# Kernel tuning notes

Measured on AMD Instinct MI355X. Metric: run time of the kernel, lower is better.

Reference implementation:

```python
import jax, jax.numpy as jnp
import numpy as np

HID = 128
SCALE = np.sqrt(HID)


def _ln(x, g, b, eps=1e-5):
    m = jnp.mean(x, axis=-1, keepdims=True)
    v = jnp.mean((x - m) ** 2, axis=-1, keepdims=True)
    return (x - m) * jax.lax.rsqrt(v + eps) * g + b


def _attention(img, txt, Wi, bi, Wt, bt, g1, b1, Wq, bq, Wk, bk, Wv, bv, g2, b2, Wo, bo):
    # img: [..., S, image_dim], txt: [..., S, text_dim] -> [..., S, HID]
    c = img @ Wi.T + bi + txt @ Wt.T + bt
    c = _ln(c, g1, b1)
    q = c @ Wq.T + bq
    k = c @ Wk.T + bk
    v = c @ Wv.T + bv
    s = jnp.einsum('...qd,...kd->...qk', q, k) / (SCALE + 1e-8)
    a = jax.nn.softmax(s, axis=-1)
    a = a + 1e-10
    a = a / jnp.sum(a, axis=-1, keepdims=True)
    a = jnp.clip(a, 1e-7, 1.0)
    ctx = jnp.einsum('...qk,...kd->...qd', a, v)
    ctx = _ln(ctx, g2, b2)
    return ctx @ Wo.T + bo


def setup_inputs() -> dict:
    key = jax.random.key(0)
    ks = jax.random.split(key, 24)
    T, Q, DI, DT = 256, 64, 2048, 768

    def xavier(k, shape):
        fan_in, fan_out = shape[1], shape[0]
        lim = np.sqrt(6.0 / (fan_in + fan_out))
        return jax.random.uniform(k, shape, jnp.float32, -lim, lim)

    return {
        'support_images': jax.random.normal(ks[0], (T, 4, DI), jnp.float32),
        'support_texts': jax.random.normal(ks[1], (T, 4, DT), jnp.float32),
        'support_labels': jax.random.randint(ks[2], (T, 4), 0, 4, jnp.int64),
        'query_images': jax.random.normal(ks[3], (T, Q, DI), jnp.float32),
        'query_texts': jax.random.normal(ks[4], (T, Q, DT), jnp.float32),
        'Wi': xavier(ks[5], (HID, DI)), 'bi': jnp.zeros((HID,)),
        'Wt': xavier(ks[6], (HID, DT)), 'bt': jnp.zeros((HID,)),
        'g1': jnp.ones((HID,)), 'b1': jnp.zeros((HID,)),
        'Wq': xavier(ks[7], (HID, HID)), 'bq': jnp.zeros((HID,)),
        'Wk': xavier(ks[8], (HID, HID)), 'bk': jnp.zeros((HID,)),
        'Wv': xavier(ks[9], (HID, HID)), 'bv': jnp.zeros((HID,)),
        'g2': jnp.ones((HID,)), 'b2': jnp.zeros((HID,)),
        'Wo': xavier(ks[10], (HID, HID)), 'bo': jnp.zeros((HID,)),
    }


def reference(support_images, support_texts, support_labels, query_images, query_texts,
              Wi, bi, Wt, bt, g1, b1, Wq, bq, Wk, bk, Wv, bv, g2, b2, Wo, bo):
    p = (Wi, bi, Wt, bt, g1, b1, Wq, bq, Wk, bk, Wv, bv, g2, b2, Wo, bo)
    # Support: attention across the 4 support items of each task -> [T, 4, HID]
    support_feats = _attention(support_images, support_texts, *p)
    # Queries: source processes each query alone (seq len 1) -> add singleton seq axis
    qf = _attention(query_images[:, :, None, :], query_texts[:, :, None, :], *p)
    qf = qf[:, :, 0, :]  # [T, Q, HID]
    # Cosine-similarity prototype scoring (eps=1e-8 as in F.cosine_similarity)
    qn = qf / jnp.clip(jnp.linalg.norm(qf, axis=-1, keepdims=True), 1e-8, None)
    pn = support_feats / jnp.clip(jnp.linalg.norm(support_feats, axis=-1, keepdims=True), 1e-8, None)
    logits = jnp.einsum('tqd,tcd->tqc', qn, pn) * 10.0  # [T, Q, 4]
    return logits
```

## Files before the change

### kernel.cpp

```cpp
#include <hip/hip_runtime.h>

typedef __bf16 bf16_t;
typedef __attribute__((ext_vector_type(4))) __bf16 bf16x4;
typedef __attribute__((ext_vector_type(8))) __bf16 bf16x8;
typedef __attribute__((ext_vector_type(4))) float floatx4;

#define LN_EPS 1e-5f

__device__ __forceinline__ void dma16(const void* g, void* l) {
    __builtin_amdgcn_global_load_lds(
        (const __attribute__((address_space(1))) void*)g,
        (__attribute__((address_space(3))) void*)l, 16, 0, 0);
}

#define WBF_WI 65536
#define WBF_WT (65536 + 262144)

__global__ __launch_bounds__(256) void k0_prep(
    const float* __restrict__ bi, const float* __restrict__ bt,
    const float* __restrict__ Wq, const float* __restrict__ Wk,
    const float* __restrict__ Wv, const float* __restrict__ Wo,
    const float* __restrict__ Wi, const float* __restrict__ Wt,
    float* __restrict__ c_all, bf16_t* __restrict__ wbf)
{
    const int b = blockIdx.x;
    if (b < 2176) {
        int i = b * 256 + threadIdx.x;
        int c4 = i & 31;
        float4 a = ((const float4*)bi)[c4];
        float4 bb = ((const float4*)bt)[c4];
        float4 v; v.x = a.x + bb.x; v.y = a.y + bb.y; v.z = a.z + bb.z; v.w = a.w + bb.w;
        ((float4*)c_all)[i] = v;
    } else {
        int i4 = (b - 2176) * 256 + threadIdx.x;
        const float* src; int dst;
        if (i4 < 16384) {
            int which = i4 >> 12, off4 = i4 & 4095;
            src = ((which == 0) ? Wq : (which == 1) ? Wk : (which == 2) ? Wv : Wo) + off4 * 4;
            dst = which * 16384 + off4 * 4;
        } else if (i4 < 16384 + 65536) {
            int off4 = i4 - 16384;
            src = Wi + off4 * 4; dst = WBF_WI + off4 * 4;
        } else {
            int off4 = i4 - (16384 + 65536);
            src = Wt + off4 * 4; dst = WBF_WT + off4 * 4;
        }
        float4 v = *(const float4*)src;
        bf16x4 pk; pk.x = (bf16_t)v.x; pk.y = (bf16_t)v.y;
                   pk.z = (bf16_t)v.z; pk.w = (bf16_t)v.w;
        *(bf16x4*)&wbf[dst] = pk;
    }
}

#define K1_MFMA8(FA0, FA1)                                                     \
    acc[0][0] = __builtin_amdgcn_mfma_f32_16x16x32_bf16(FA0, fb0, acc[0][0], 0, 0, 0); \
    acc[0][1] = __builtin_amdgcn_mfma_f32_16x16x32_bf16(FA0, fb1, acc[0][1], 0, 0, 0); \
    acc[0][2] = __builtin_amdgcn_mfma_f32_16x16x32_bf16(FA0, fb2, acc[0][2], 0, 0, 0); \
    acc[0][3] = __builtin_amdgcn_mfma_f32_16x16x32_bf16(FA0, fb3, acc[0][3], 0, 0, 0); \
    acc[1][0] = __builtin_amdgcn_mfma_f32_16x16x32_bf16(FA1, fb0, acc[1][0], 0, 0, 0); \
    acc[1][1] = __builtin_amdgcn_mfma_f32_16x16x32_bf16(FA1, fb1, acc[1][1], 0, 0, 0); \
    acc[1][2] = __builtin_amdgcn_mfma_f32_16x16x32_bf16(FA1, fb2, acc[1][2], 0, 0, 0); \
    acc[1][3] = __builtin_amdgcn_mfma_f32_16x16x32_bf16(FA1, fb3, acc[1][3], 0, 0, 0);

#define K1_BODY(A0, A1, B0, B1, B2, B3, K)                                     \
    {                                                                          \
        float4 p00 = *(const float4*)((A0) + (K));                             \
        float4 p01 = *(const float4*)((A0) + (K) + 4);                         \
        float4 p10 = *(const float4*)((A1) + (K));                             \
        float4 p11 = *(const float4*)((A1) + (K) + 4);                         \
        bf16x8 fb0 = *(const bf16x8*)((B0) + (K));                             \
        bf16x8 fb1 = *(const bf16x8*)((B1) + (K));                             \
        bf16x8 fb2 = *(const bf16x8*)((B2) + (K));                             \
        bf16x8 fb3 = *(const bf16x8*)((B3) + (K));                             \
        bf16x8 fa0, fa1;                                                       \
        fa0[0] = (bf16_t)p00.x; fa0[1] = (bf16_t)p00.y;                        \
        fa0[2] = (bf16_t)p00.z; fa0[3] = (bf16_t)p00.w;                        \
        fa0[4] = (bf16_t)p01.x; fa0[5] = (bf16_t)p01.y;                        \
        fa0[6] = (bf16_t)p01.z; fa0[7] = (bf16_t)p01.w;                        \
        fa1[0] = (bf16_t)p10.x; fa1[1] = (bf16_t)p10.y;                        \
        fa1[2] = (bf16_t)p10.z; fa1[3] = (bf16_t)p10.w;                        \
        fa1[4] = (bf16_t)p11.x; fa1[5] = (bf16_t)p11.y;                        \
        fa1[6] = (bf16_t)p11.z; fa1[7] = (bf16_t)p11.w;                        \
        K1_MFMA8(fa0, fa1)                                                     \
    }

__global__ __launch_bounds__(256, 4) void k1_gemm(
    const float* __restrict__ qimg, const float* __restrict__ qtxt,
    const float* __restrict__ simg, const float* __restrict__ stxt,
    const bf16_t* __restrict__ wbf, float* __restrict__ c_all)
{
    const bf16_t* Wib = wbf + WBF_WI;
    const bf16_t* Wtb = wbf + WBF_WT;

    const int tid  = threadIdx.x;
    const int m0   = blockIdx.x * 64;
    const int chnk = blockIdx.y;
    const bool isq = (m0 < 16384);
    const int rb   = isq ? m0 : (m0 - 16384);
    const float* Aimg = isq ? qimg : simg;
    const float* Atxt = isq ? qtxt : stxt;

    const int wid  = tid >> 6;
    const int lane = tid & 63;
    const int quad = lane >> 4;
    const int l16  = lane & 15;
    const int wr   = wid >> 1;
    const int wc   = wid & 1;

    const int ar0 = rb + wr * 32 + l16;
    const int bc0 = wc * 64 + l16;

    floatx4 acc[2][4];
#pragma unroll
    for (int i = 0; i < 2; ++i)
#pragma unroll
        for (int j = 0; j < 4; ++j) acc[i][j] = (floatx4)0.f;

    const int kb = chnk * 704;
    const int ke = kb + 704;

    const int ie = (ke < 2048) ? ke : 2048;
    if (kb < ie) {
        const float*  a0 = Aimg + (size_t)ar0 * 2048 + quad * 8 + kb;
        const float*  a1 = a0 + (size_t)16 * 2048;
        const bf16_t* b0 = Wib + (size_t)bc0 * 2048 + quad * 8 + kb;
        const bf16_t* b1 = b0 + (size_t)16 * 2048;
        const bf16_t* b2 = b0 + (size_t)32 * 2048;
        const bf16_t* b3 = b0 + (size_t)48 * 2048;
        const int n = ie - kb;
#pragma unroll 2
        for (int k = 0; k < n; k += 32) K1_BODY(a0, a1, b0, b1, b2, b3, k)
    }
    const int ts = (kb > 2048) ? kb : 2048;
    if (ts < ke) {
        const int off = ts - 2048;
        const float*  a0 = Atxt + (size_t)ar0 * 768 + quad * 8 + off;
        const float*  a1 = a0 + (size_t)16 * 768;
        const bf16_t* b0 = Wtb + (size_t)bc0 * 768 + quad * 8 + off;
        const bf16_t* b1 = b0 + (size_t)16 * 768;
        const bf16_t* b2 = b0 + (size_t)32 * 768;
        const bf16_t* b3 = b0 + (size_t)48 * 768;
        const int n = ke - ts;
#pragma unroll 2
        for (int k = 0; k < n; k += 32) K1_BODY(a0, a1, b0, b1, b2, b3, k)
    }

#pragma unroll
    for (int nt = 0; nt < 4; ++nt) {
        int col = wc * 64 + nt * 16 + l16;
#pragma unroll
        for (int mt = 0; mt < 2; ++mt)
#pragma unroll
            for (int r = 0; r < 4; ++r) {
                int row = wr * 32 + mt * 16 + quad * 4 + r;
                unsafeAtomicAdd(&c_all[(size_t)(m0 + row) * 128 + col], acc[mt][nt][r]);
            }
    }
}

#define K2_ST 136

__global__ __launch_bounds__(256) void k2_fused(
    const float* __restrict__ c_all, const bf16_t* __restrict__ wbf,
    const float* __restrict__ bq, const float* __restrict__ bk,
    const float* __restrict__ bv, const float* __restrict__ bo,
    const float* __restrict__ g1, const float* __restrict__ b1,
    const float* __restrict__ g2, const float* __restrict__ b2,
    float* __restrict__ out)
{
    __shared__ bf16_t tT[64 * K2_ST];
    __shared__ bf16_t tW[128 * 128];
    __shared__ float  cs[4][128];
    __shared__ float  qkv[3][4][128];
    __shared__ float  att[4][4];
    __shared__ float  pl[4][132];

    const int tid  = threadIdx.x;
    const int wid  = tid >> 6;
    const int lane = tid & 63;
    const int quad = lane >> 4;
    const int l16  = lane & 15;
    const int task = blockIdx.x;
    const int t0   = task * 64;
    const int r0   = wid * 16;
    const int jr4  = lane >> 4;
    const int jp   = lane & 15;

#pragma unroll
    for (int ii = 0; ii < 8; ++ii) {
        int i = 8 * wid + ii;
        int row = 4 * i + jr4;
        int c = jp ^ (row & 15);
        dma16(wbf + 0 * 16384 + row * 128 + c * 8, (char*)tW + i * 1024);
    }

    float bvr[8], g2r[8], b2r[8], bor[8];
#pragma unroll
    for (int nt = 0; nt < 8; ++nt) {
        int col = nt * 16 + l16;
        bvr[nt] = bv[col]; g2r[nt] = g2[col]; b2r[nt] = b2[col]; bor[nt] = bo[col];
    }

    {
        const int g8 = lane >> 3, s8 = lane & 7;
        float g1a[16], b1a[16];
#pragma unroll
        for (int mm = 0; mm < 4; ++mm) {
            *(float4*)&g1a[mm * 4] = ((const float4*)(g1 + s8 * 16))[mm];
            *(float4*)&b1a[mm * 4] = ((const float4*)(b1 + s8 * 16))[mm];
        }
#pragma unroll
        for (int p = 0; p < 2; ++p) {
            int rloc = r0 + p * 8 + g8;
            const float* src = c_all + (size_t)(t0 + rloc) * 128 + s8 * 16;
            float v[16];
#pragma unroll
            for (int mm = 0; mm < 4; ++mm) *(float4*)&v[mm * 4] = ((const float4*)src)[mm];
            float s = 0.f, q = 0.f;
#pragma unroll
            for (int m = 0; m < 16; ++m) { s += v[m]; q += v[m] * v[m]; }
#pragma unroll
            for (int m = 1; m < 8; m <<= 1) { s += __shfl_xor(s, m); q += __shfl_xor(q, m); }
            float mean = s * (1.f / 128.f);
            float var  = q * (1.f / 128.f) - mean * mean;
            float rs   = rsqrtf(var + LN_EPS);
            bf16x8 o0, o1;
#pragma unroll
            for (int m = 0; m < 8; ++m) o0[m] = (bf16_t)((v[m] - mean) * rs * g1a[m] + b1a[m]);
#pragma unroll
            for (int m = 0; m < 8; ++m) o1[m] = (bf16_t)((v[8 + m] - mean) * rs * g1a[8 + m] + b1a[8 + m]);
            *(bf16x8*)&tT[rloc * K2_ST + s8 * 16]     = o0;
            *(bf16x8*)&tT[rloc * K2_ST + s8 * 16 + 8] = o1;
        }
    }
    {
        const float* src = c_all + (size_t)(16384 + task * 4 + wid) * 128;
        float x0 = src[lane], x1 = src[64 + lane];
        float s = x0 + x1, q = x0 * x0 + x1 * x1;
#pragma unroll
        for (int m = 1; m < 64; m <<= 1) { s += __shfl_xor(s, m); q += __shfl_xor(q, m); }
        float mean = s * (1.f / 128.f);
        float var  = q * (1.f / 128.f) - mean * mean;
        float rs   = rsqrtf(var + LN_EPS);
        cs[wid][lane]      = (x0 - mean) * rs * g1[lane] + b1[lane];
        cs[wid][64 + lane] = (x1 - mean) * rs * g1[64 + lane] + b1[64 + lane];
    }
    __syncthreads();

#pragma unroll
    for (int j = 0; j < 2; ++j) {
        int o = tid + j * 256, s = o >> 7, n = o & 127;
        const float4* c4 = (const float4*)cs[s];
        float acc = 0.f;
#pragma unroll
        for (int c = 0; c < 16; ++c) {
            bf16x8 wv = *(const bf16x8*)&tW[n * 128 + ((c ^ (n & 15)) << 3)];
            float4 a0 = c4[c * 2], a1 = c4[c * 2 + 1];
            acc += a0.x * (float)wv[0] + a0.y * (float)wv[1]
                 + a0.z * (float)wv[2] + a0.w * (float)wv[3]
                 + a1.x * (float)wv[4] + a1.y * (float)wv[5]
                 + a1.z * (float)wv[6] + a1.w * (float)wv[7];
        }
        qkv[0][s][n] = acc + bq[n];
    }
    __syncthreads();
#pragma unroll
    for (int ii = 0; ii < 8; ++ii) {
        int i = 8 * wid + ii;
        int row = 4 * i + jr4;
        int c = jp ^ (row & 15);
        dma16(wbf + 1 * 16384 + row * 128 + c * 8, (char*)tW + i * 1024);
    }
    __syncthreads();
#pragma unroll
    for (int j = 0; j < 2; ++j) {
        int o = tid + j * 256, s = o >> 7, n = o & 127;
        const float4* c4 = (const float4*)cs[s];
        float acc = 0.f;
#pragma unroll
        for (int c = 0; c < 16; ++c) {
            bf16x8 wv = *(const bf16x8*)&tW[n * 128 + ((c ^ (n & 15)) << 3)];
            float4 a0 = c4[c * 2], a1 = c4[c * 2 + 1];
            acc += a0.x * (float)wv[0] + a0.y * (float)wv[1]
                 + a0.z * (float)wv[2] + a0.w * (float)wv[3]
                 + a1.x * (float)wv[4] + a1.y * (float)wv[5]
                 + a1.z * (float)wv[6] + a1.w * (float)wv[7];
        }
        qkv[1][s][n] = acc + bk[n];
    }
    __syncthreads();
#pragma unroll
    for (int ii = 0; ii < 8; ++ii) {
        int i = 8 * wid + ii;
        int row = 4 * i + jr4;
        int c = jp ^ (row & 15);
        dma16(wbf + 2 * 16384 + row * 128 + c * 8, (char*)tW + i * 1024);
    }
    __syncthreads();

    floatx4 acc[8];
#pragma unroll
    for (int nt = 0; nt < 8; ++nt) acc[nt] = (floatx4)0.f;
#pragma unroll
    for (int ks = 0; ks < 4; ++ks) {
        bf16x8 a = *(const bf16x8*)&tT[(r0 + l16) * K2_ST + ks * 32 + quad * 8];
#pragma unroll
        for (int nt = 0; nt < 8; ++nt) {
            bf16x8 b = *(const bf16x8*)&tW[(nt * 16 + l16) * 128 + (((ks * 4 + quad) ^ l16) << 3)];
            acc[nt] = __builtin_amdgcn_mfma_f32_16x16x32_bf16(a, b, acc[nt], 0, 0, 0);
        }
    }
#pragma unroll
    for (int nt = 0; nt < 8; ++nt)
#pragma unroll
        for (int r = 0; r < 4; ++r) acc[nt][r] += bvr[nt];

#pragma unroll
    for (int j = 0; j < 2; ++j) {
        int o = tid + j * 256, s = o >> 7, n = o & 127;
        const float4* c4 = (const float4*)cs[s];
        float a = 0.f;
#pragma unroll
        for (int c = 0; c < 16; ++c) {
            bf16x8 wv = *(const bf16x8*)&tW[n * 128 + ((c ^ (n & 15)) << 3)];
            float4 a0 = c4[c * 2], a1 = c4[c * 2 + 1];
            a += a0.x * (float)wv[0] + a0.y * (float)wv[1]
               + a0.z * (float)wv[2] + a0.w * (float)wv[3]
               + a1.x * (float)wv[4] + a1.y * (float)wv[5]
               + a1.z * (float)wv[6] + a1.w * (float)wv[7];
        }
        qkv[2][s][n] = a + bv[n];
    }
    if (tid < 16) {
        int i = tid >> 2, j = tid & 3;
        const float4* qv = (const float4*)qkv[0][i];
        const float4* kv = (const float4*)qkv[1][j];
        float a = 0.f;
#pragma unroll
        for (int k = 0; k < 32; ++k) {
            float4 x = qv[k], y = kv[k];
            a += x.x * y.x + x.y * y.y + x.z * y.z + x.w * y.w;
        }
        att[i][j] = a * (float)(1.0 / (11.313708498984761 + 1e-8));
    }
#pragma unroll
    for (int r = 0; r < 4; ++r) {
        float s = 0.f, q = 0.f;
#pragma unroll
        for (int nt = 0; nt < 8; ++nt) { float x = acc[nt][r]; s += x; q += x * x; }
#pragma unroll
        for (int m = 1; m < 16; m <<= 1) { s += __shfl_xor(s, m); q += __shfl_xor(q, m); }
        float mean = s * (1.f / 128.f);
        float var  = q * (1.f / 128.f) - mean * mean;
        float rs   = rsqrtf(var + LN_EPS);
        int row = r0 + quad * 4 + r;
#pragma unroll
        for (int nt = 0; nt < 8; ++nt)
            tT[row * K2_ST + nt * 16 + l16] = (bf16_t)((acc[nt][r] - mean) * rs * g2r[nt] + b2r[nt]);
    }
    __syncthreads();
#pragma unroll
    for (int ii = 0; ii < 8; ++ii) {
        int i = 8 * wid + ii;
        int row = 4 * i + jr4;
        int c = jp ^ (row & 15);
        dma16(wbf + 3 * 16384 + row * 128 + c * 8, (char*)tW + i * 1024);
    }
    if (tid < 4) {
        float s0 = att[tid][0], s1 = att[tid][1], s2 = att[tid][2], s3 = att[tid][3];
        float m = fmaxf(fmaxf(s0, s1), fmaxf(s2, s3));
        float e0 = expf(s0 - m), e1 = expf(s1 - m), e2 = expf(s2 - m), e3 = expf(s3 - m);
        float se = e0 + e1 + e2 + e3;
        float a0 = e0 / se + 1e-10f, a1 = e1 / se + 1e-10f;
        float a2 = e2 / se + 1e-10f, a3 = e3 / se + 1e-10f;
        float t = a0 + a1 + a2 + a3;
        att[tid][0] = fminf(fmaxf(a0 / t, 1e-7f), 1.f);
        att[tid][1] = fminf(fmaxf(a1 / t, 1e-7f), 1.f);
        att[tid][2] = fminf(fmaxf(a2 / t, 1e-7f), 1.f);
        att[tid][3] = fminf(fmaxf(a3 / t, 1e-7f), 1.f);
    }
    __syncthreads();

#pragma unroll
    for (int j = 0; j < 2; ++j) {
        int o = tid + j * 256, s = o >> 7, n = o & 127;
        qkv[0][s][n] = att[s][0] * qkv[2][0][n] + att[s][1] * qkv[2][1][n]
                     + att[s][2] * qkv[2][2][n] + att[s][3] * qkv[2][3][n];
    }
    __syncthreads();
    {
        float x0 = qkv[0][wid][lane], x1 = qkv[0][wid][64 + lane];
        float s = x0 + x1, q = x0 * x0 + x1 * x1;
#pragma unroll
        for (int m = 1; m < 64; m <<= 1) { s += __shfl_xor(s, m); q += __shfl_xor(q, m); }
        float mean = s * (1.f / 128.f);
        float var  = q * (1.f / 128.f) - mean * mean;
        float rs   = rsqrtf(var + LN_EPS);
        cs[wid][lane]      = (x0 - mean) * rs * g2[lane] + b2[lane];
        cs[wid][64 + lane] = (x1 - mean) * rs * g2[64 + lane] + b2[64 + lane];
    }
    __syncthreads();

#pragma unroll
    for (int j = 0; j < 2; ++j) {
        int o = tid + j * 256, s = o >> 7, n = o & 127;
        const float4* c4 = (const float4*)cs[s];
        float a = 0.f;
#pragma unroll
        for (int c = 0; c < 16; ++c) {
            bf16x8 wv = *(const bf16x8*)&tW[n * 128 + ((c ^ (n & 15)) << 3)];
            float4 a0 = c4[c * 2], a1 = c4[c * 2 + 1];
            a += a0.x * (float)wv[0] + a0.y * (float)wv[1]
               + a0.z * (float)wv[2] + a0.w * (float)wv[3]
               + a1.x * (float)wv[4] + a1.y * (float)wv[5]
               + a1.z * (float)wv[6] + a1.w * (float)wv[7];
        }
        qkv[1][s][n] = a + bo[n];
    }

    floatx4 acc2[8];
#pragma unroll
    for (int nt = 0; nt < 8; ++nt) acc2[nt] = (floatx4)0.f;
#pragma unroll
    for (int ks = 0; ks < 4; ++ks) {
        bf16x8 a = *(const bf16x8*)&tT[(r0 + l16) * K2_ST + ks * 32 + quad * 8];
#pragma unroll
        for (int nt = 0; nt < 8; ++nt) {
            bf16x8 b = *(const bf16x8*)&tW[(nt * 16 + l16) * 128 + (((ks * 4 + quad) ^ l16) << 3)];
            acc2[nt] = __builtin_amdgcn_mfma_f32_16x16x32_bf16(a, b, acc2[nt], 0, 0, 0);
        }
    }
    __syncthreads();
    {
        float x0 = qkv[1][wid][lane], x1 = qkv[1][wid][64 + lane];
        float q = x0 * x0 + x1 * x1;
#pragma unroll
        for (int m = 1; m < 64; m <<= 1) q += __shfl_xor(q, m);
        float inv = 1.f / fmaxf(sqrtf(q), 1e-8f);
        pl[wid][lane]      = x0 * inv;
        pl[wid][64 + lane] = x1 * inv;
    }
    __syncthreads();

#pragma unroll
    for (int r = 0; r < 4; ++r) {
        float st[8]; float q = 0.f;
#pragma unroll
        for (int nt = 0; nt < 8; ++nt) {
            float x = acc2[nt][r] + bor[nt]; st[nt] = x; q += x * x;
        }
#pragma unroll
        for (int m = 1; m < 16; m <<= 1) q += __shfl_xor(q, m);
        float inv = 1.f / fmaxf(sqrtf(q), 1e-8f);
        float d0 = 0.f, d1 = 0.f, d2 = 0.f, d3 = 0.f;
#pragma unroll
        for (int nt = 0; nt < 8; ++nt) {
            float xn = st[nt] * inv;
            int col = nt * 16 + l16;
            d0 += xn * pl[0][col]; d1 += xn * pl[1][col];
            d2 += xn * pl[2][col]; d3 += xn * pl[3][col];
        }
#pragma unroll
        for (int m = 1; m < 16; m <<= 1) {
            d0 += __shfl_xor(d0, m); d1 += __shfl_xor(d1, m);
            d2 += __shfl_xor(d2, m); d3 += __shfl_xor(d3, m);
        }
        if (l16 == 0) {
            int qi = r0 + quad * 4 + r;
            float* o = out + (size_t)task * 256 + qi * 4;
            o[0] = d0 * 10.f; o[1] = d1 * 10.f; o[2] = d2 * 10.f; o[3] = d3 * 10.f;
        }
    }
}

extern "C" void kernel_launch(void* const* d_in, const int* in_sizes, int n_in,
                              void* d_out, int out_size, void* d_ws, size_t ws_size,
                              hipStream_t stream)
{
    const float* simg = (const float*)d_in[0];
    const float* stxt = (const float*)d_in[1];
    const float* qimg = (const float*)d_in[3];
    const float* qtxt = (const float*)d_in[4];
    const float* Wi = (const float*)d_in[5];
    const float* bi = (const float*)d_in[6];
    const float* Wt = (const float*)d_in[7];
    const float* bt = (const float*)d_in[8];
    const float* g1 = (const float*)d_in[9];
    const float* b1 = (const float*)d_in[10];
    const float* Wq = (const float*)d_in[11];
    const float* bq = (const float*)d_in[12];
    const float* Wk = (const float*)d_in[13];
    const float* bk = (const float*)d_in[14];
    const float* Wv = (const float*)d_in[15];
    const float* bv = (const float*)d_in[16];
    const float* g2 = (const float*)d_in[17];
    const float* b2 = (const float*)d_in[18];
    const float* Wo = (const float*)d_in[19];
    const float* bo = (const float*)d_in[20];
    float* out = (float*)d_out;

    float*  c_all = (float*)d_ws;
    bf16_t* wbf   = (bf16_t*)(c_all + (size_t)17408 * 128);

    k0_prep<<<2592, 256, 0, stream>>>(bi, bt, Wq, Wk, Wv, Wo, Wi, Wt, c_all, wbf);
    k1_gemm<<<dim3(272, 4), 256, 0, stream>>>(qimg, qtxt, simg, stxt, wbf, c_all);
    k2_fused<<<256, 256, 0, stream>>>(c_all, wbf, bq, bk, bv, bo, g1, b1, g2, b2, out);
}
```

Baseline: 360.0 us.

## Stage k1 GEMM tiles through LDS and split fused tail into three kernels

The input-projection GEMM now loads 64-wide K slabs of activations and weights cooperatively with coalesced global loads, converts them to bf16 into padded LDS tiles, and prefetches the next slab into registers while MFMAs consume the current one. Previously each lane read strided rows straight from global memory. The support path moves out of the per-task kernel: an MFMA-based Q/K/V kernel, a per-task attention kernel that writes normalized prototypes, and a query kernel that reads them. This swaps scalar dot-product loops for tensor-core work on the support side, at the cost of two extra launches and extra global round trips for qkv and prototypes.

```diff
diff --git a/kernel.cpp b/kernel.cpp
--- a/kernel.cpp
+++ b/kernel.cpp
@@ -52,36 +52,25 @@
     }
 }
 
-#define K1_MFMA8(FA0, FA1)                                                     \
-    acc[0][0] = __builtin_amdgcn_mfma_f32_16x16x32_bf16(FA0, fb0, acc[0][0], 0, 0, 0); \
-    acc[0][1] = __builtin_amdgcn_mfma_f32_16x16x32_bf16(FA0, fb1, acc[0][1], 0, 0, 0); \
-    acc[0][2] = __builtin_amdgcn_mfma_f32_16x16x32_bf16(FA0, fb2, acc[0][2], 0, 0, 0); \
-    acc[0][3] = __builtin_amdgcn_mfma_f32_16x16x32_bf16(FA0, fb3, acc[0][3], 0, 0, 0); \
-    acc[1][0] = __builtin_amdgcn_mfma_f32_16x16x32_bf16(FA1, fb0, acc[1][0], 0, 0, 0); \
-    acc[1][1] = __builtin_amdgcn_mfma_f32_16x16x32_bf16(FA1, fb1, acc[1][1], 0, 0, 0); \
-    acc[1][2] = __builtin_amdgcn_mfma_f32_16x16x32_bf16(FA1, fb2, acc[1][2], 0, 0, 0); \
-    acc[1][3] = __builtin_amdgcn_mfma_f32_16x16x32_bf16(FA1, fb3, acc[1][3], 0, 0, 0);
-
-#define K1_BODY(A0, A1, B0, B1, B2, B3, K)                                     \
+#define K1_LD 72
+
+#define K1_LOAD(K0)                                                            \
     {                                                                          \
-        float4 p00 = *(const float4*)((A0) + (K));                             \
-        float4 p01 = *(const float4*)((A0) + (K) + 4);                         \
-        float4 p10 = *(const float4*)((A1) + (K));                             \
-        float4 p11 = *(const float4*)((A1) + (K) + 4);                         \
-        bf16x8 fb0 = *(const bf16x8*)((B0) + (K));                             \
-        bf16x8 fb1 = *(const bf16x8*)((B1) + (K));                             \
-        bf16x8 fb2 = *(const bf16x8*)((B2) + (K));                             \
-        bf16x8 fb3 = *(const bf16x8*)((B3) + (K));                             \
-        bf16x8 fa0, fa1;                                                       \
-        fa0[0] = (bf16_t)p00.x; fa0[1] = (bf16_t)p00.y;                        \
-        fa0[2] = (bf16_t)p00.z; fa0[3] = (bf16_t)p00.w;                        \
-        fa0[4] = (bf16_t)p01.x; fa0[5] = (bf16_t)p01.y;                        \
-        fa0[6] = (bf16_t)p01.z; fa0[7] = (bf16_t)p01.w;                        \
-        fa1[0] = (bf16_t)p10.x; fa1[1] = (bf16_t)p10.y;                        \
-        fa1[2] = (bf16_t)p10.z; fa1[3] = (bf16_t)p10.w;                        \
-        fa1[4] = (bf16_t)p11.x; fa1[5] = (bf16_t)p11.y;                        \
-        fa1[6] = (bf16_t)p11.z; fa1[7] = (bf16_t)p11.w;                        \
-        K1_MFMA8(fa0, fa1)                                                     \
+        const int k0_ = (K0);                                                  \
+        const float* ab_; const bf16_t* bb_; int lda_, ldb_;                   \
+        if (k0_ < 2048) {                                                      \
+            ab_ = Aimg + (size_t)rb * 2048 + k0_; lda_ = 2048;                 \
+            bb_ = Wib + k0_; ldb_ = 2048;                                      \
+        } else {                                                               \
+            ab_ = Atxt + (size_t)rb * 768 + (k0_ - 2048); lda_ = 768;          \
+            bb_ = Wtb + (k0_ - 2048); ldb_ = 768;                              \
+        }                                                                      \
+        _Pragma("unroll")                                                      \
+        for (int p = 0; p < 4; ++p)                                            \
+            aR[p] = *(const float4*)(ab_ + (size_t)(16 * p + arow) * lda_ + acol); \
+        _Pragma("unroll")                                                      \
+        for (int p = 0; p < 4; ++p)                                            \
+            bR[p] = *(const bf16x8*)(bb_ + (size_t)(32 * p + brow) * ldb_ + bcol); \
     }
 
 __global__ __launch_bounds__(256, 4) void k1_gemm(
@@ -89,6 +78,9 @@
     const float* __restrict__ simg, const float* __restrict__ stxt,
     const bf16_t* __restrict__ wbf, float* __restrict__ c_all)
 {
+    __shared__ bf16_t lA[64 * K1_LD];
+    __shared__ bf16_t lB[128 * K1_LD];
+
     const bf16_t* Wib = wbf + WBF_WI;
     const bf16_t* Wtb = wbf + WBF_WT;
 
@@ -107,8 +99,13 @@
     const int wr   = wid >> 1;
     const int wc   = wid & 1;
 
-    const int ar0 = rb + wr * 32 + l16;
-    const int bc0 = wc * 64 + l16;
+    const int arow = tid >> 4;
+    const int acol = (tid & 15) << 2;
+    const int brow = tid >> 3;
+    const int bcol = (tid & 7) << 3;
+
+    float4 aR[4];
+    bf16x8 bR[4];
 
     floatx4 acc[2][4];
 #pragma unroll
@@ -117,32 +114,38 @@
         for (int j = 0; j < 4; ++j) acc[i][j] = (floatx4)0.f;
 
     const int kb = chnk * 704;
-    const int ke = kb + 704;
-
-    const int ie = (ke < 2048) ? ke : 2048;
-    if (kb < ie) {
-        const float*  a0 = Aimg + (size_t)ar0 * 2048 + quad * 8 + kb;
-        const float*  a1 = a0 + (size_t)16 * 2048;
-        const bf16_t* b0 = Wib + (size_t)bc0 * 2048 + quad * 8 + kb;
-        const bf16_t* b1 = b0 + (size_t)16 * 2048;
-        const bf16_t* b2 = b0 + (size_t)32 * 2048;
-        const bf16_t* b3 = b0 + (size_t)48 * 2048;
-        const int n = ie - kb;
-#pragma unroll 2
-        for (int k = 0; k < n; k += 32) K1_BODY(a0, a1, b0, b1, b2, b3, k)
-    }
-    const int ts = (kb > 2048) ? kb : 2048;
-    if (ts < ke) {
-        const int off = ts - 2048;
-        const float*  a0 = Atxt + (size_t)ar0 * 768 + quad * 8 + off;
-        const float*  a1 = a0 + (size_t)16 * 768;
-        const bf16_t* b0 = Wtb + (size_t)bc0 * 768 + quad * 8 + off;
-        const bf16_t* b1 = b0 + (size_t)16 * 768;
-        const bf16_t* b2 = b0 + (size_t)32 * 768;
-        const bf16_t* b3 = b0 + (size_t)48 * 768;
-        const int n = ke - ts;
-#pragma unroll 2
-        for (int k = 0; k < n; k += 32) K1_BODY(a0, a1, b0, b1, b2, b3, k)
+
+    K1_LOAD(kb)
+    for (int s = 0; s < 11; ++s) {
+        __syncthreads();
+#pragma unroll
+        for (int p = 0; p < 4; ++p) {
+            bf16x4 pk; pk.x = (bf16_t)aR[p].x; pk.y = (bf16_t)aR[p].y;
+                       pk.z = (bf16_t)aR[p].z; pk.w = (bf16_t)aR[p].w;
+            *(bf16x4*)&lA[(16 * p + arow) * K1_LD + acol] = pk;
+        }
+#pragma unroll
+        for (int p = 0; p < 4; ++p)
+            *(bf16x8*)&lB[(32 * p + brow) * K1_LD + bcol] = bR[p];
+        __syncthreads();
+        if (s + 1 < 11) K1_LOAD(kb + (s + 1) * 64)
+
+#pragma unroll
+        for (int ks = 0; ks < 2; ++ks) {
+            bf16x8 af[2], bf[4];
+#pragma unroll
+            for (int mt = 0; mt < 2; ++mt)
+                af[mt] = *(const bf16x8*)&lA[(wr * 32 + mt * 16 + l16) * K1_LD + ks * 32 + quad * 8];
+#pragma unroll
+            for (int nt = 0; nt < 4; ++nt)
+                bf[nt] = *(const bf16x8*)&lB[(wc * 64 + nt * 16 + l16) * K1_LD + ks * 32 + quad * 8];
+#pragma unroll
+            for (int mt = 0; mt < 2; ++mt)
+#pragma unroll
+                for (int nt = 0; nt < 4; ++nt)
+                    acc[mt][nt] = __builtin_amdgcn_mfma_f32_16x16x32_bf16(
+                        af[mt], bf[nt], acc[mt][nt], 0, 0, 0);
+        }
     }
 
 #pragma unroll
@@ -160,28 +163,23 @@
 
 #define K2_ST 136
 
-__global__ __launch_bounds__(256) void k2_fused(
+__global__ __launch_bounds__(256) void ks1_qkv(
     const float* __restrict__ c_all, const bf16_t* __restrict__ wbf,
     const float* __restrict__ bq, const float* __restrict__ bk,
-    const float* __restrict__ bv, const float* __restrict__ bo,
+    const float* __restrict__ bv,
     const float* __restrict__ g1, const float* __restrict__ b1,
-    const float* __restrict__ g2, const float* __restrict__ b2,
-    float* __restrict__ out)
+    float* __restrict__ qkvs)
 {
     __shared__ bf16_t tT[64 * K2_ST];
     __shared__ bf16_t tW[128 * 128];
-    __shared__ float  cs[4][128];
-    __shared__ float  qkv[3][4][128];
-    __shared__ float  att[4][4];
-    __shared__ float  pl[4][132];
 
     const int tid  = threadIdx.x;
     const int wid  = tid >> 6;
     const int lane = tid & 63;
     const int quad = lane >> 4;
     const int l16  = lane & 15;
-    const int task = blockIdx.x;
-    const int t0   = task * 64;
+    const int bm   = blockIdx.x;
+    const int w    = blockIdx.y;
     const int r0   = wid * 16;
     const int jr4  = lane >> 4;
     const int jp   = lane & 15;
@@ -191,15 +189,13 @@
         int i = 8 * wid + ii;
         int row = 4 * i + jr4;
         int c = jp ^ (row & 15);
-        dma16(wbf + 0 * 16384 + row * 128 + c * 8, (char*)tW + i * 1024);
-    }
-
-    float bvr[8], g2r[8], b2r[8], bor[8];
-#pragma unroll
-    for (int nt = 0; nt < 8; ++nt) {
-        int col = nt * 16 + l16;
-        bvr[nt] = bv[col]; g2r[nt] = g2[col]; b2r[nt] = b2[col]; bor[nt] = bo[col];
-    }
+        dma16(wbf + w * 16384 + row * 128 + c * 8, (char*)tW + i * 1024);
+    }
+
+    const float* Bw = (w == 0) ? bq : (w == 1) ? bk : bv;
+    float bwr[8];
+#pragma unroll
+    for (int nt = 0; nt < 8; ++nt) bwr[nt] = Bw[nt * 16 + l16];
 
     {
         const int g8 = lane >> 3, s8 = lane & 7;
@@ -212,7 +208,7 @@
 #pragma unroll
         for (int p = 0; p < 2; ++p) {
             int rloc = r0 + p * 8 + g8;
-            const float* src = c_all + (size_t)(t0 + rloc) * 128 + s8 * 16;
+            const float* src = c_all + (size_t)(16384 + bm * 64 + rloc) * 128 + s8 * 16;
             float v[16];
 #pragma unroll
             for (int mm = 0; mm < 4; ++mm) *(float4*)&v[mm * 4] = ((const float4*)src)[mm];
@@ -233,69 +229,6 @@
             *(bf16x8*)&tT[rloc * K2_ST + s8 * 16 + 8] = o1;
         }
     }
-    {
-        const float* src = c_all + (size_t)(16384 + task * 4 + wid) * 128;
-        float x0 = src[lane], x1 = src[64 + lane];
-        float s = x0 + x1, q = x0 * x0 + x1 * x1;
-#pragma unroll
-        for (int m = 1; m < 64; m <<= 1) { s += __shfl_xor(s, m); q += __shfl_xor(q, m); }
-        float mean = s * (1.f / 128.f);
-        float var  = q * (1.f / 128.f) - mean * mean;
-        float rs   = rsqrtf(var + LN_EPS);
-        cs[wid][lane]      = (x0 - mean) * rs * g1[lane] + b1[lane];
-        cs[wid][64 + lane] = (x1 - mean) * rs * g1[64 + lane] + b1[64 + lane];
-    }
-    __syncthreads();
-
-#pragma unroll
-    for (int j = 0; j < 2; ++j) {
-        int o = tid + j * 256, s = o >> 7, n = o & 127;
-        const float4* c4 = (const float4*)cs[s];
-        float acc = 0.f;
-#pragma unroll
-        for (int c = 0; c < 16; ++c) {
-            bf16x8 wv = *(const bf16x8*)&tW[n * 128 + ((c ^ (n & 15)) << 3)];
-            float4 a0 = c4[c * 2], a1 = c4[c * 2 + 1];
-            acc += a0.x * (float)wv[0] + a0.y * (float)wv[1]
-                 + a0.z * (float)wv[2] + a0.w * (float)wv[3]
-                 + a1.x * (float)wv[4] + a1.y * (float)wv[5]
-                 + a1.z * (float)wv[6] + a1.w * (float)wv[7];
-        }
-        qkv[0][s][n] = acc + bq[n];
-    }
-    __syncthreads();
-#pragma unroll
-    for (int ii = 0; ii < 8; ++ii) {
-        int i = 8 * wid + ii;
-        int row = 4 * i + jr4;
-        int c = jp ^ (row & 15);
-        dma16(wbf + 1 * 16384 + row * 128 + c * 8, (char*)tW + i * 1024);
-    }
-    __syncthreads();
-#pragma unroll
-    for (int j = 0; j < 2; ++j) {
-        int o = tid + j * 256, s = o >> 7, n = o & 127;
-        const float4* c4 = (const float4*)cs[s];
-        float acc = 0.f;
-#pragma unroll
-        for (int c = 0; c < 16; ++c) {
-            bf16x8 wv = *(const bf16x8*)&tW[n * 128 + ((c ^ (n & 15)) << 3)];
-            float4 a0 = c4[c * 2], a1 = c4[c * 2 + 1];
-            acc += a0.x * (float)wv[0] + a0.y * (float)wv[1]
-                 + a0.z * (float)wv[2] + a0.w * (float)wv[3]
-                 + a1.x * (float)wv[4] + a1.y * (float)wv[5]
-                 + a1.z * (float)wv[6] + a1.w * (float)wv[7];
-        }
-        qkv[1][s][n] = acc + bk[n];
-    }
-    __syncthreads();
-#pragma unroll
-    for (int ii = 0; ii < 8; ++ii) {
-        int i = 8 * wid + ii;
-        int row = 4 * i + jr4;
-        int c = jp ^ (row & 15);
-        dma16(wbf + 2 * 16384 + row * 128 + c * 8, (char*)tW + i * 1024);
-    }
     __syncthreads();
 
     floatx4 acc[8];
@@ -311,54 +244,34 @@
         }
     }
 #pragma unroll
-    for (int nt = 0; nt < 8; ++nt)
-#pragma unroll
-        for (int r = 0; r < 4; ++r) acc[nt][r] += bvr[nt];
-
-#pragma unroll
-    for (int j = 0; j < 2; ++j) {
-        int o = tid + j * 256, s = o >> 7, n = o & 127;
-        const float4* c4 = (const float4*)cs[s];
-        float a = 0.f;
-#pragma unroll
-        for (int c = 0; c < 16; ++c) {
-            bf16x8 wv = *(const bf16x8*)&tW[n * 128 + ((c ^ (n & 15)) << 3)];
-            float4 a0 = c4[c * 2], a1 = c4[c * 2 + 1];
-            a += a0.x * (float)wv[0] + a0.y * (float)wv[1]
-               + a0.z * (float)wv[2] + a0.w * (float)wv[3]
-               + a1.x * (float)wv[4] + a1.y * (float)wv[5]
-               + a1.z * (float)wv[6] + a1.w * (float)wv[7];
-        }
-        qkv[2][s][n] = a + bv[n];
-    }
-    if (tid < 16) {
-        int i = tid >> 2, j = tid & 3;
-        const float4* qv = (const float4*)qkv[0][i];
-        const float4* kv = (const float4*)qkv[1][j];
-        float a = 0.f;
-#pragma unroll
-        for (int k = 0; k < 32; ++k) {
-            float4 x = qv[k], y = kv[k];
-            a += x.x * y.x + x.y * y.y + x.z * y.z + x.w * y.w;
-        }
-        att[i][j] = a * (float)(1.0 / (11.313708498984761 + 1e-8));
-    }
-#pragma unroll
-    for (int r = 0; r < 4; ++r) {
-        float s = 0.f, q = 0.f;
-#pragma unroll
-        for (int nt = 0; nt < 8; ++nt) { float x = acc[nt][r]; s += x; q += x * x; }
-#pragma unroll
-        for (int m = 1; m < 16; m <<= 1) { s += __shfl_xor(s, m); q += __shfl_xor(q, m); }
-        float mean = s * (1.f / 128.f);
-        float var  = q * (1.f / 128.f) - mean * mean;
-        float rs   = rsqrtf(var + LN_EPS);
-        int row = r0 + quad * 4 + r;
-#pragma unroll
-        for (int nt = 0; nt < 8; ++nt)
-            tT[row * K2_ST + nt * 16 + l16] = (bf16_t)((acc[nt][r] - mean) * rs * g2r[nt] + b2r[nt]);
-    }
-    __syncthreads();
+    for (int nt = 0; nt < 8; ++nt) {
+        int col = nt * 16 + l16;
+#pragma unroll
+        for (int r = 0; r < 4; ++r) {
+            int row = bm * 64 + r0 + quad * 4 + r;
+            qkvs[(size_t)w * 131072 + (size_t)row * 128 + col] = acc[nt][r] + bwr[nt];
+        }
+    }
+}
+
+__global__ __launch_bounds__(256) void ks2_attn(
+    const float* __restrict__ qkvs, const bf16_t* __restrict__ wbf,
+    const float* __restrict__ bo,
+    const float* __restrict__ g2, const float* __restrict__ b2,
+    float* __restrict__ pn)
+{
+    __shared__ bf16_t tW[128 * 128];
+    __shared__ float  q_[4][128], k_[4][128], v_[4][128];
+    __shared__ float  att[4][4];
+    __shared__ float  cs[4][128], cx[4][128];
+
+    const int tid  = threadIdx.x;
+    const int wid  = tid >> 6;
+    const int lane = tid & 63;
+    const int task = blockIdx.x;
+    const int jr4  = lane >> 4;
+    const int jp   = lane & 15;
+
 #pragma unroll
     for (int ii = 0; ii < 8; ++ii) {
         int i = 8 * wid + ii;
@@ -366,6 +279,29 @@
         int c = jp ^ (row & 15);
         dma16(wbf + 3 * 16384 + row * 128 + c * 8, (char*)tW + i * 1024);
     }
+#pragma unroll
+    for (int j = 0; j < 2; ++j) {
+        int o = tid + j * 256, s = o >> 7, n = o & 127;
+        size_t base = (size_t)(task * 4 + s) * 128 + n;
+        q_[s][n] = qkvs[base];
+        k_[s][n] = qkvs[131072 + base];
+        v_[s][n] = qkvs[262144 + base];
+    }
+    __syncthreads();
+
+    if (tid < 16) {
+        int i = tid >> 2, j = tid & 3;
+        const float4* qv = (const float4*)q_[i];
+        const float4* kv = (const float4*)k_[j];
+        float a = 0.f;
+#pragma unroll
+        for (int k = 0; k < 32; ++k) {
+            float4 x = qv[k], y = kv[k];
+            a += x.x * y.x + x.y * y.y + x.z * y.z + x.w * y.w;
+        }
+        att[i][j] = a * (float)(1.0 / (11.313708498984761 + 1e-8));
+    }
+    __syncthreads();
     if (tid < 4) {
         float s0 = att[tid][0], s1 = att[tid][1], s2 = att[tid][2], s3 = att[tid][3];
         float m = fmaxf(fmaxf(s0, s1), fmaxf(s2, s3));
@@ -380,16 +316,15 @@
         att[tid][3] = fminf(fmaxf(a3 / t, 1e-7f), 1.f);
     }
     __syncthreads();
-
 #pragma unroll
     for (int j = 0; j < 2; ++j) {
         int o = tid + j * 256, s = o >> 7, n = o & 127;
-        qkv[0][s][n] = att[s][0] * qkv[2][0][n] + att[s][1] * qkv[2][1][n]
-                     + att[s][2] * qkv[2][2][n] + att[s][3] * qkv[2][3][n];
+        cx[s][n] = att[s][0] * v_[0][n] + att[s][1] * v_[1][n]
+                 + att[s][2] * v_[2][n] + att[s][3] * v_[3][n];
     }
     __syncthreads();
     {
-        float x0 = qkv[0][wid][lane], x1 = qkv[0][wid][64 + lane];
+        float x0 = cx[wid][lane], x1 = cx[wid][64 + lane];
         float s = x0 + x1, q = x0 * x0 + x1 * x1;
 #pragma unroll
         for (int m = 1; m < 64; m <<= 1) { s += __shfl_xor(s, m); q += __shfl_xor(q, m); }
@@ -400,7 +335,6 @@
         cs[wid][64 + lane] = (x1 - mean) * rs * g2[64 + lane] + b2[64 + lane];
     }
     __syncthreads();
-
 #pragma unroll
     for (int j = 0; j < 2; ++j) {
         int o = tid + j * 256, s = o >> 7, n = o & 127;
@@ -415,8 +349,137 @@
                + a1.x * (float)wv[4] + a1.y * (float)wv[5]
                + a1.z * (float)wv[6] + a1.w * (float)wv[7];
         }
-        qkv[1][s][n] = a + bo[n];
-    }
+        cx[s][n] = a + bo[n];
+    }
+    __syncthreads();
+    {
+        float x0 = cx[wid][lane], x1 = cx[wid][64 + lane];
+        float q = x0 * x0 + x1 * x1;
+#pragma unroll
+        for (int m = 1; m < 64; m <<= 1) q += __shfl_xor(q, m);
+        float inv = 1.f / fmaxf(sqrtf(q), 1e-8f);
+        float* dst = pn + (size_t)(task * 4 + wid) * 128;
+        dst[lane]      = x0 * inv;
+        dst[64 + lane] = x1 * inv;
+    }
+}
+
+__global__ __launch_bounds__(256) void kq_query(
+    const float* __restrict__ c_all, const bf16_t* __restrict__ wbf,
+    const float* __restrict__ bv, const float* __restrict__ bo,
+    const float* __restrict__ g1, const float* __restrict__ b1,
+    const float* __restrict__ g2, const float* __restrict__ b2,
+    const float* __restrict__ pn, float* __restrict__ out)
+{
+    __shared__ bf16_t tT[64 * K2_ST];
+    __shared__ bf16_t tW[128 * 128];
+    __shared__ float  pl[4][132];
+
+    const int tid  = threadIdx.x;
+    const int wid  = tid >> 6;
+    const int lane = tid & 63;
+    const int quad = lane >> 4;
+    const int l16  = lane & 15;
+    const int task = blockIdx.x;
+    const int t0   = task * 64;
+    const int r0   = wid * 16;
+    const int jr4  = lane >> 4;
+    const int jp   = lane & 15;
+
+#pragma unroll
+    for (int ii = 0; ii < 8; ++ii) {
+        int i = 8 * wid + ii;
+        int row = 4 * i + jr4;
+        int c = jp ^ (row & 15);
+        dma16(wbf + 2 * 16384 + row * 128 + c * 8, (char*)tW + i * 1024);
+    }
+    if (tid < 128) {
+        int r = tid >> 5, c4 = tid & 31;
+        *(float4*)&pl[r][c4 * 4] = *(const float4*)(pn + ((size_t)task * 4 + r) * 128 + c4 * 4);
+    }
+
+    float bvr[8], g2r[8], b2r[8], bor[8];
+#pragma unroll
+    for (int nt = 0; nt < 8; ++nt) {
+        int col = nt * 16 + l16;
+        bvr[nt] = bv[col]; g2r[nt] = g2[col]; b2r[nt] = b2[col]; bor[nt] = bo[col];
+    }
+
+    {
+        const int g8 = lane >> 3, s8 = lane & 7;
+        float g1a[16], b1a[16];
+#pragma unroll
+        for (int mm = 0; mm < 4; ++mm) {
+            *(float4*)&g1a[mm * 4] = ((const float4*)(g1 + s8 * 16))[mm];
+            *(float4*)&b1a[mm * 4] = ((const float4*)(b1 + s8 * 16))[mm];
+        }
+#pragma unroll
+        for (int p = 0; p < 2; ++p) {
+            int rloc = r0 + p * 8 + g8;
+            const float* src = c_all + (size_t)(t0 + rloc) * 128 + s8 * 16;
+            float v[16];
+#pragma unroll
+            for (int mm = 0; mm < 4; ++mm) *(float4*)&v[mm * 4] = ((const float4*)src)[mm];
+            float s = 0.f, q = 0.f;
+#pragma unroll
+            for (int m = 0; m < 16; ++m) { s += v[m]; q += v[m] * v[m]; }
+#pragma unroll
+            for (int m = 1; m < 8; m <<= 1) { s += __shfl_xor(s, m); q += __shfl_xor(q, m); }
+            float mean = s * (1.f / 128.f);
+            float var  = q * (1.f / 128.f) - mean * mean;
+            float rs   = rsqrtf(var + LN_EPS);
+            bf16x8 o0, o1;
+#pragma unroll
+            for (int m = 0; m < 8; ++m) o0[m] = (bf16_t)((v[m] - mean) * rs * g1a[m] + b1a[m]);
+#pragma unroll
+            for (int m = 0; m < 8; ++m) o1[m] = (bf16_t)((v[8 + m] - mean) * rs * g1a[8 + m] + b1a[8 + m]);
+            *(bf16x8*)&tT[rloc * K2_ST + s8 * 16]     = o0;
+            *(bf16x8*)&tT[rloc * K2_ST + s8 * 16 + 8] = o1;
+        }
+    }
+    __syncthreads();
+
+    floatx4 acc[8];
+#pragma unroll
+    for (int nt = 0; nt < 8; ++nt) acc[nt] = (floatx4)0.f;
+#pragma unroll
+    for (int ks = 0; ks < 4; ++ks) {
+        bf16x8 a = *(const bf16x8*)&tT[(r0 + l16) * K2_ST + ks * 32 + quad * 8];
+#pragma unroll
+        for (int nt = 0; nt < 8; ++nt) {
+            bf16x8 b = *(const bf16x8*)&tW[(nt * 16 + l16) * 128 + (((ks * 4 + quad) ^ l16) << 3)];
+            acc[nt] = __builtin_amdgcn_mfma_f32_16x16x32_bf16(a, b, acc[nt], 0, 0, 0);
+        }
+    }
+#pragma unroll
+    for (int nt = 0; nt < 8; ++nt)
+#pragma unroll
+        for (int r = 0; r < 4; ++r) acc[nt][r] += bvr[nt];
+
+#pragma unroll
+    for (int r = 0; r < 4; ++r) {
+        float s = 0.f, q = 0.f;
+#pragma unroll
+        for (int nt = 0; nt < 8; ++nt) { float x = acc[nt][r]; s += x; q += x * x; }
+#pragma unroll
+        for (int m = 1; m < 16; m <<= 1) { s += __shfl_xor(s, m); q += __shfl_xor(q, m); }
+        float mean = s * (1.f / 128.f);
+        float var  = q * (1.f / 128.f) - mean * mean;
+        float rs   = rsqrtf(var + LN_EPS);
+        int row = r0 + quad * 4 + r;
+#pragma unroll
+        for (int nt = 0; nt < 8; ++nt)
+            tT[row * K2_ST + nt * 16 + l16] = (bf16_t)((acc[nt][r] - mean) * rs * g2r[nt] + b2r[nt]);
+    }
+    __syncthreads();
+#pragma unroll
+    for (int ii = 0; ii < 8; ++ii) {
+        int i = 8 * wid + ii;
+        int row = 4 * i + jr4;
+        int c = jp ^ (row & 15);
+        dma16(wbf + 3 * 16384 + row * 128 + c * 8, (char*)tW + i * 1024);
+    }
+    __syncthreads();
 
     floatx4 acc2[8];
 #pragma unroll
@@ -430,17 +493,6 @@
             acc2[nt] = __builtin_amdgcn_mfma_f32_16x16x32_bf16(a, b, acc2[nt], 0, 0, 0);
         }
     }
-    __syncthreads();
-    {
-        float x0 = qkv[1][wid][lane], x1 = qkv[1][wid][64 + lane];
-        float q = x0 * x0 + x1 * x1;
-#pragma unroll
-        for (int m = 1; m < 64; m <<= 1) q += __shfl_xor(q, m);
-        float inv = 1.f / fmaxf(sqrtf(q), 1e-8f);
-        pl[wid][lane]      = x0 * inv;
-        pl[wid][64 + lane] = x1 * inv;
-    }
-    __syncthreads();
 
 #pragma unroll
     for (int r = 0; r < 4; ++r) {
@@ -501,8 +553,12 @@
 
     float*  c_all = (float*)d_ws;
     bf16_t* wbf   = (bf16_t*)(c_all + (size_t)17408 * 128);
+    float*  qkvs  = (float*)(wbf + 425984);
+    float*  pn    = qkvs + (size_t)3 * 131072;
 
     k0_prep<<<2592, 256, 0, stream>>>(bi, bt, Wq, Wk, Wv, Wo, Wi, Wt, c_all, wbf);
     k1_gemm<<<dim3(272, 4), 256, 0, stream>>>(qimg, qtxt, simg, stxt, wbf, c_all);
-    k2_fused<<<256, 256, 0, stream>>>(c_all, wbf, bq, bk, bv, bo, g1, b1, g2, b2, out);
-}
+    ks1_qkv<<<dim3(16, 3), 256, 0, stream>>>(c_all, wbf, bq, bk, bv, g1, b1, qkvs);
+    ks2_attn<<<256, 256, 0, stream>>>(qkvs, wbf, bo, g2, b2, pn);
+    kq_query<<<256, 256, 0, stream>>>(c_all, wbf, bv, bo, g1, b1, g2, b2, pn, out);
+}
```

Result: faster. 311.8 us (-13.4%).
